# Kernel optimization log

Measured on AMD Instinct MI355X. Metric: run time of the kernel, lower is better.

Reference implementation:

```python
import jax, jax.numpy as jnp
import numpy as np

B, D_IN, D, E = 65536, 512, 512, 8  # batch, input dim, node hidden dim, n_children (=decision dim)


def setup_inputs() -> dict:
    key = jax.random.key(0)
    ks = jax.random.split(key, 5)
    s = 0.02  # weight init scale
    return {
        "x": jax.random.normal(ks[0], (B, D_IN), jnp.float32),
        "W_root": jax.random.normal(ks[1], (D_IN, D), jnp.float32) * s,
        "b_root": jnp.zeros((D,), jnp.float32),
        "W_dec": jax.random.normal(ks[2], (D, E), jnp.float32) * s,
        "b_dec": jnp.zeros((E,), jnp.float32),
        "W_leaf": jax.random.normal(ks[3], (E, D, D), jnp.float32) * s,
        "b_leaf": jnp.zeros((E, D), jnp.float32),
        "W_ldec": jax.random.normal(ks[4], (E, D, E), jnp.float32) * s,
        "b_ldec": jnp.zeros((E, E), jnp.float32),
    }


def reference(x, W_root, b_root, W_dec, b_dec, W_leaf, b_leaf, W_ldec, b_ldec):
    # Root node (Dense+relu), flatten is a no-op on [B, D]
    h = jax.nn.relu(x @ W_root + b_root)                                 # [B, D]
    dec = jax.nn.softmax(h @ W_dec + b_dec, axis=-1)                     # [B, E] root decision (softmax, outputDim>1)
    route = jnp.argmax(dec, axis=-1)                                     # [B] hard routing
    # Leaf children: each leaf applies its own node Dense+relu and decision Dense+softmax.
    # Dense reference for the boolean-mask dispatch/combine: compute all experts on all
    # samples, then gather each sample's routed expert output (math-equivalent to the
    # original gather-per-mask + concat + reorder-gather, since partitions are disjoint).
    lh = jax.nn.relu(jnp.einsum('bd,edh->ebh', h, W_leaf) + b_leaf[:, None, :])     # [E, B, D]
    ldec = jax.nn.softmax(jnp.einsum('ebd,edo->ebo', lh, W_ldec) + b_ldec[:, None, :], axis=-1)  # [E, B, E]
    sel = jnp.take_along_axis(ldec.transpose(1, 0, 2), route[:, None, None], axis=1)[:, 0]  # [B, E]
    # concat root decisionOut [B,1,E] with ordered leaf outputs [B,1,E] along axis -2
    return jnp.concatenate([dec[:, None, :], sel[:, None, :]], axis=1)  # [B, 2, E]
```

## Files before the change

### kernel.cpp

```cpp
#include <hip/hip_runtime.h>
#include <stdint.h>

#define DD   512
#define EE   8

typedef __bf16 bf16x8 __attribute__((ext_vector_type(8)));
typedef float  f32x4  __attribute__((ext_vector_type(4)));
typedef unsigned short u16x8 __attribute__((ext_vector_type(8)));

__device__ __forceinline__ unsigned short f2bf(float f) {
    union { float f; unsigned int i; } v; v.f = f;
    unsigned int x = v.i;
    x += 0x7fffu + ((x >> 16) & 1u);
    return (unsigned short)(x >> 16);
}
__device__ __forceinline__ void gload_lds16(const void* g, void* l) {
    __builtin_amdgcn_global_load_lds(
        (const __attribute__((address_space(1))) unsigned int*)g,
        (__attribute__((address_space(3))) unsigned int*)l, 16, 0, 0);
}
__device__ __forceinline__ f32x4 mfma_bf16(bf16x8 a, bf16x8 b, f32x4 c) {
    return __builtin_amdgcn_mfma_f32_16x16x32_bf16(a, b, c, 0, 0, 0);
}

__global__ __launch_bounds__(256) void k_wtr(
    const float* __restrict__ W_root, unsigned short* __restrict__ WrTh)
{
    __shared__ unsigned short tile[64][65];
    int tl = blockIdx.x, tr = tl >> 3, tc = tl & 7;
    int t = threadIdx.x;
    #pragma unroll
    for (int j = 0; j < 16; j++) {
        int i2 = t + j * 256; int r = i2 >> 6, c = i2 & 63;
        tile[r][c] = f2bf(W_root[(size_t)(tr * 64 + r) * DD + tc * 64 + c]);
    }
    __syncthreads();
    #pragma unroll
    for (int j = 0; j < 16; j++) {
        int i2 = t + j * 256; int r = i2 >> 6, c = i2 & 63;
        WrTh[(size_t)(tc * 64 + r) * DD + tr * 64 + c] = tile[c][r];
    }
}

__global__ __launch_bounds__(256) void k_trW(
    const float* __restrict__ W_leaf, unsigned short* __restrict__ WlT)
{
    __shared__ unsigned short tile[64][65];
    int bid = blockIdx.x;
    int e = bid >> 6;
    int tl = bid & 63, tr = tl >> 3, tc = tl & 7;
    const float* src = W_leaf + (size_t)e * DD * DD;
    unsigned short* dst = WlT + (size_t)e * DD * DD;
    int t = threadIdx.x;
    #pragma unroll
    for (int j = 0; j < 16; j++) {
        int i2 = t + j * 256; int r = i2 >> 6, c = i2 & 63;
        tile[r][c] = f2bf(src[(size_t)(tr * 64 + r) * DD + tc * 64 + c]);
    }
    __syncthreads();
    #pragma unroll
    for (int j = 0; j < 16; j++) {
        int i2 = t + j * 256; int r = i2 >> 6, c = i2 & 63;
        dst[(size_t)(tc * 64 + r) * DD + tr * 64 + c] = tile[c][r];
    }
}

__global__ __launch_bounds__(256) void k_trpad(
    const float* __restrict__ W_ldec, unsigned short* __restrict__ WldT)
{
    int idx = blockIdx.x * 256 + threadIdx.x;
    int e = idx >> 13, rem = idx & 8191;
    int o = rem >> 9, k = rem & 511;
    unsigned short v = 0;
    if (o < 8) v = f2bf(W_ldec[((size_t)e * DD + k) * EE + o]);
    WldT[idx] = v;
}

__global__ __launch_bounds__(256) void k_trdec(
    const float* __restrict__ W_dec, unsigned short* __restrict__ WdT)
{
    int idx = blockIdx.x * 256 + threadIdx.x;
    int o = idx >> 9, k = idx & 511;
    WdT[idx] = (o < 8) ? f2bf(W_dec[(size_t)k * EE + o]) : (unsigned short)0;
}

__global__ __launch_bounds__(256) void k_root(
    const float* __restrict__ x,
    const unsigned short* __restrict__ WrTh,
    const float* __restrict__ b_root,
    const unsigned short* __restrict__ WdT,
    unsigned short* __restrict__ hbuf,
    float* __restrict__ logit_part)
{
    __shared__ unsigned short smem[128 * 136];
    unsigned short* lsA = smem;
    unsigned short* lsB = smem + 4096;

    int bid = blockIdx.x;
    int mb = (bid >> 5) * 8 + (bid & 7);
    int cb = (bid >> 3) & 3;
    int m0 = mb * 128, n0 = cb * 128;

    int t = threadIdx.x;
    int wid = t >> 6, lane = t & 63;
    int wr = wid >> 1, wc = wid & 1;
    int l15 = lane & 15, l4 = lane >> 4;

    int ar = t >> 1, ah16 = (t & 1) * 16;
    const float* pA = x + (size_t)(m0 + ar) * DD + ah16;
    const unsigned short* srcB0 = WrTh + (size_t)(n0 + (t >> 2)) * DD + (t & 3) * 8;
    const unsigned short* srcB1 = srcB0 + (size_t)64 * DD;
    unsigned short* dB0 = &lsB[t * 8];
    unsigned short* dB1 = &lsB[2048 + t * 8];

    f32x4 acc[4][4];
    #pragma unroll
    for (int m = 0; m < 4; m++)
        #pragma unroll
        for (int n = 0; n < 4; n++) acc[m][n] = (f32x4){0.f, 0.f, 0.f, 0.f};

    for (int k0 = 0; k0 < DD; k0 += 32) {
        const float4* pAv = (const float4*)(pA + k0);
        float4 v0 = pAv[0], v1 = pAv[1], v2 = pAv[2], v3 = pAv[3];
        float vv[16] = {v0.x,v0.y,v0.z,v0.w, v1.x,v1.y,v1.z,v1.w,
                        v2.x,v2.y,v2.z,v2.w, v3.x,v3.y,v3.z,v3.w};
        bf16x8 hv0, hv1;
        #pragma unroll
        for (int j = 0; j < 8; j++) { hv0[j] = (__bf16)vv[j]; hv1[j] = (__bf16)vv[8 + j]; }
        __syncthreads();
        *(bf16x8*)&lsA[ar * 32 + ah16]     = hv0;
        *(bf16x8*)&lsA[ar * 32 + ah16 + 8] = hv1;
        gload_lds16(srcB0 + k0, dB0);
        gload_lds16(srcB1 + k0, dB1);
        __syncthreads();

        bf16x8 fa[4], fb[4];
        #pragma unroll
        for (int m = 0; m < 4; m++)
            fa[m] = *(const bf16x8*)&lsA[(wr * 64 + m * 16 + l15) * 32 + l4 * 8];
        #pragma unroll
        for (int n = 0; n < 4; n++)
            fb[n] = *(const bf16x8*)&lsB[(wc * 64 + n * 16 + l15) * 32 + l4 * 8];
        #pragma unroll
        for (int m = 0; m < 4; m++)
            #pragma unroll
            for (int n = 0; n < 4; n++)
                acc[m][n] = mfma_bf16(fa[m], fb[n], acc[m][n]);
    }
    __syncthreads();

    float bcol[4];
    #pragma unroll
    for (int n = 0; n < 4; n++) bcol[n] = b_root[n0 + wc * 64 + n * 16 + l15];
    #pragma unroll
    for (int n = 0; n < 4; n++) {
        int coll = wc * 64 + n * 16 + l15;
        #pragma unroll
        for (int m = 0; m < 4; m++) {
            int rl = wr * 64 + m * 16 + l4 * 4;
            #pragma unroll
            for (int i = 0; i < 4; i++) {
                float v = acc[m][n][i] + bcol[n];
                v = v > 0.f ? v : 0.f;
                smem[(rl + i) * 136 + coll] = f2bf(v);
            }
        }
    }
    __syncthreads();

    {
        int r = t >> 1, c0 = (t & 1) * 64;
        unsigned short* dst = hbuf + (size_t)(m0 + r) * DD + n0 + c0;
        #pragma unroll
        for (int j = 0; j < 8; j++)
            *(u16x8*)(dst + j * 8) = *(const u16x8*)&smem[r * 136 + c0 + j * 8];
    }

    f32x4 acc2[2];
    acc2[0] = (f32x4){0.f, 0.f, 0.f, 0.f};
    acc2[1] = (f32x4){0.f, 0.f, 0.f, 0.f};
    #pragma unroll
    for (int kk = 0; kk < 4; kk++) {
        bf16x8 bb = *(const bf16x8*)(WdT + (size_t)l15 * DD + n0 + kk * 32 + l4 * 8);
        #pragma unroll
        for (int m2 = 0; m2 < 2; m2++) {
            bf16x8 aa = *(const bf16x8*)&smem[(wid * 32 + m2 * 16 + l15) * 136 + kk * 32 + l4 * 8];
            acc2[m2] = mfma_bf16(aa, bb, acc2[m2]);
        }
    }
    if (l15 < 8) {
        #pragma unroll
        for (int m2 = 0; m2 < 2; m2++)
            #pragma unroll
            for (int i = 0; i < 4; i++) {
                int rowg = m0 + wid * 32 + m2 * 16 + l4 * 4 + i;
                logit_part[((size_t)cb * 65536 + rowg) * 8 + l15] = acc2[m2][i];
            }
    }
}

__global__ __launch_bounds__(256) void k_dec(
    const float* __restrict__ logit_part,
    const float* __restrict__ b_dec,
    float* __restrict__ out,
    int* __restrict__ route,
    int* __restrict__ meta,
    int* __restrict__ rescue_list)
{
    int b = blockIdx.x * 256 + threadIdx.x;
    double lg[8];
    #pragma unroll
    for (int o = 0; o < 8; o++) lg[o] = (double)b_dec[o];
    #pragma unroll
    for (int ppp = 0; ppp < 4; ppp++) {
        #pragma unroll
        for (int o = 0; o < 8; o++)
            lg[o] += (double)logit_part[((size_t)ppp * 65536 + b) * 8 + o];
    }
    double mx = -1e300, mx2 = -1e300; int idx = 0;
    #pragma unroll
    for (int o = 0; o < 8; o++) {
        if (lg[o] > mx) { mx2 = mx; mx = lg[o]; idx = o; }
        else if (lg[o] > mx2) mx2 = lg[o];
    }
    float ev[8], s = 0.f;
    #pragma unroll
    for (int o = 0; o < 8; o++) { ev[o] = expf((float)(lg[o] - mx)); s += ev[o]; }
    float inv = 1.f / s;
    float4 o0, o1;
    o0.x = ev[0]*inv; o0.y = ev[1]*inv; o0.z = ev[2]*inv; o0.w = ev[3]*inv;
    o1.x = ev[4]*inv; o1.y = ev[5]*inv; o1.z = ev[6]*inv; o1.w = ev[7]*inv;
    float4* op = (float4*)(out + (size_t)b * 16);
    op[0] = o0; op[1] = o1;
    route[b] = idx;
    if (mx - mx2 < 3e-3) {
        int pos = atomicAdd(&meta[27], 1);
        if (pos < 8192) rescue_list[pos] = b;
    }
}

__global__ __launch_bounds__(256) void k_rescue(
    const float* __restrict__ x,
    const float* __restrict__ W_root,
    const float* __restrict__ b_root,
    const float* __restrict__ W_dec,
    const float* __restrict__ b_dec,
    const int* __restrict__ rescue_list,
    const int* __restrict__ meta,
    float* __restrict__ out,
    int* __restrict__ route)
{
    int nresc = min(meta[27], 8192);
    if ((int)blockIdx.x >= nresc) return;
    int row = rescue_list[blockIdx.x];
    int t = threadIdx.x;

    __shared__ float xr[512];
    __shared__ double red[4][8];
    xr[t * 2]     = x[(size_t)row * DD + t * 2];
    xr[t * 2 + 1] = x[(size_t)row * DD + t * 2 + 1];
    __syncthreads();

    int d0 = t, d1 = t + 256;
    double a0 = 0.0, a1 = 0.0;
    for (int k = 0; k < DD; k++) {
        double xv = (double)xr[k];
        a0 += xv * (double)W_root[(size_t)k * DD + d0];
        a1 += xv * (double)W_root[(size_t)k * DD + d1];
    }
    double h0 = fmax(a0 + (double)b_root[d0], 0.0);
    double h1 = fmax(a1 + (double)b_root[d1], 0.0);
    double so[8];
    #pragma unroll
    for (int o = 0; o < 8; o++)
        so[o] = h0 * (double)W_dec[d0 * 8 + o] + h1 * (double)W_dec[d1 * 8 + o];
    #pragma unroll
    for (int d = 1; d < 64; d <<= 1)
        #pragma unroll
        for (int o = 0; o < 8; o++) so[o] += __shfl_xor(so[o], d, 64);
    if ((t & 63) == 0) {
        #pragma unroll
        for (int o = 0; o < 8; o++) red[t >> 6][o] = so[o];
    }
    __syncthreads();
    if (t == 0) {
        double lg[8]; double mx = -1e300; int idx = 0;
        #pragma unroll
        for (int o = 0; o < 8; o++) {
            lg[o] = red[0][o] + red[1][o] + red[2][o] + red[3][o] + (double)b_dec[o];
            if (lg[o] > mx) { mx = lg[o]; idx = o; }
        }
        double ev[8], s = 0.0;
        #pragma unroll
        for (int o = 0; o < 8; o++) { ev[o] = exp(lg[o] - mx); s += ev[o]; }
        double inv = 1.0 / s;
        float4 o0, o1;
        o0.x = (float)(ev[0]*inv); o0.y = (float)(ev[1]*inv);
        o0.z = (float)(ev[2]*inv); o0.w = (float)(ev[3]*inv);
        o1.x = (float)(ev[4]*inv); o1.y = (float)(ev[5]*inv);
        o1.z = (float)(ev[6]*inv); o1.w = (float)(ev[7]*inv);
        float4* op = (float4*)(out + (size_t)row * 16);
        op[0] = o0; op[1] = o1;
        route[row] = idx;
    }
}

__global__ __launch_bounds__(256) void k_count(
    const int* __restrict__ route, int* __restrict__ meta)
{
    __shared__ int wcnt[4][8];
    int b = blockIdx.x * 256 + threadIdx.x;
    int e = route[b];
    int lane = threadIdx.x & 63, wv = threadIdx.x >> 6;
    #pragma unroll
    for (int ex = 0; ex < 8; ex++) {
        unsigned long long m = __ballot(e == ex);
        if (lane == 0) wcnt[wv][ex] = __popcll(m);
    }
    __syncthreads();
    if (threadIdx.x < 8) {
        int ex = threadIdx.x;
        atomicAdd(&meta[ex], wcnt[0][ex] + wcnt[1][ex] + wcnt[2][ex] + wcnt[3][ex]);
    }
}

__global__ void k_scan(int* __restrict__ meta)
{
    if (threadIdx.x == 0 && blockIdx.x == 0) {
        int run = 0, rb = 0;
        for (int e = 0; e < 8; e++) {
            int c = meta[e];
            meta[16 + e] = run;
            meta[8 + e]  = run;
            int n = (c + 127) >> 7;
            for (int j = 0; j < n; j++) meta[32 + rb + j] = e | (j << 8);
            rb += n;
            run += n << 7;
        }
        meta[24] = rb;
    }
}

__global__ __launch_bounds__(256) void k_scatter(
    const int* __restrict__ route, int* __restrict__ meta, int* __restrict__ rows_list)
{
    __shared__ int wcnt[4][8];
    __shared__ int wbase[4][8];
    int b = blockIdx.x * 256 + threadIdx.x;
    int e = route[b];
    int lane = threadIdx.x & 63, wv = threadIdx.x >> 6;
    unsigned long long mymask = 0;
    #pragma unroll
    for (int ex = 0; ex < 8; ex++) {
        unsigned long long m = __ballot(e == ex);
        if (e == ex) mymask = m;
        if (lane == 0) wcnt[wv][ex] = __popcll(m);
    }
    int myrank = __popcll(mymask & ((1ULL << lane) - 1ULL));
    __syncthreads();
    if (threadIdx.x < 8) {
        int ex = threadIdx.x;
        int c0 = wcnt[0][ex], c1 = wcnt[1][ex], c2 = wcnt[2][ex], c3 = wcnt[3][ex];
        int base = atomicAdd(&meta[8 + ex], c0 + c1 + c2 + c3);
        wbase[0][ex] = base;
        wbase[1][ex] = base + c0;
        wbase[2][ex] = base + c0 + c1;
        wbase[3][ex] = base + c0 + c1 + c2;
    }
    __syncthreads();
    rows_list[wbase[wv][e] + myrank] = b;
}

__global__ __launch_bounds__(256) void k_gemm2(
    const unsigned short* __restrict__ hbuf,
    const unsigned short* __restrict__ WlT,
    const float* __restrict__ b_leaf,
    const unsigned short* __restrict__ WldT,
    const int* __restrict__ rows_list,
    const int* __restrict__ meta,
    float* __restrict__ ldec_part)
{
    __shared__ unsigned short lsA[128 * 32];
    __shared__ unsigned short lsB[128 * 32];
    __shared__ unsigned short lh[128 * 136];

    int bid = blockIdx.x;
    int rbid = (bid >> 5) * 8 + (bid & 7);
    int cb = (bid >> 3) & 3;
    if (rbid >= meta[24]) return;
    int pk = meta[32 + rbid];
    int e = pk & 255, lrb = pk >> 8;
    int poff_e = meta[16 + e], cnt_e = meta[e];
    int n0 = cb * 128;

    int t = threadIdx.x;
    int wid = t >> 6, lane = t & 63;
    int wr = wid >> 1, wc = wid & 1;
    int l15 = lane & 15, l4 = lane >> 4;

    int slot0 = poff_e + lrb * 128 + (t >> 2);
    int slot1 = slot0 + 64;
    int lastv = poff_e + cnt_e - 1;
    int grow0 = rows_list[min(slot0, lastv)];
    int grow1 = rows_list[min(slot1, lastv)];
    const unsigned short* srcA0 = hbuf + (size_t)grow0 * DD + (t & 3) * 8;
    const unsigned short* srcA1 = hbuf + (size_t)grow1 * DD + (t & 3) * 8;
    const unsigned short* srcB0 = WlT + (size_t)e * DD * DD + (size_t)(n0 + (t >> 2)) * DD + (t & 3) * 8;
    const unsigned short* srcB1 = srcB0 + (size_t)64 * DD;
    unsigned short* dA0 = &lsA[t * 8];
    unsigned short* dA1 = &lsA[2048 + t * 8];
    unsigned short* dB0 = &lsB[t * 8];
    unsigned short* dB1 = &lsB[2048 + t * 8];

    f32x4 acc[4][4];
    #pragma unroll
    for (int m = 0; m < 4; m++)
        #pragma unroll
        for (int n = 0; n < 4; n++) acc[m][n] = (f32x4){0.f, 0.f, 0.f, 0.f};

    for (int k0 = 0; k0 < DD; k0 += 32) {
        __syncthreads();
        gload_lds16(srcA0 + k0, dA0);
        gload_lds16(srcA1 + k0, dA1);
        gload_lds16(srcB0 + k0, dB0);
        gload_lds16(srcB1 + k0, dB1);
        __syncthreads();
        bf16x8 af[4], bfr[4];
        #pragma unroll
        for (int m = 0; m < 4; m++)
            af[m] = *(const bf16x8*)&lsA[(wr * 64 + m * 16 + l15) * 32 + l4 * 8];
        #pragma unroll
        for (int n = 0; n < 4; n++)
            bfr[n] = *(const bf16x8*)&lsB[(wc * 64 + n * 16 + l15) * 32 + l4 * 8];
        #pragma unroll
        for (int m = 0; m < 4; m++)
            #pragma unroll
            for (int n = 0; n < 4; n++)
                acc[m][n] = mfma_bf16(af[m], bfr[n], acc[m][n]);
    }

    #pragma unroll
    for (int n = 0; n < 4; n++) {
        int coll = wc * 64 + n * 16 + l15;
        float bv = b_leaf[(size_t)e * DD + n0 + coll];
        #pragma unroll
        for (int m = 0; m < 4; m++) {
            int rl = wr * 64 + m * 16 + l4 * 4;
            #pragma unroll
            for (int i = 0; i < 4; i++) {
                float v = acc[m][n][i] + bv;
                v = v > 0.f ? v : 0.f;
                lh[(rl + i) * 136 + coll] = f2bf(v);
            }
        }
    }
    __syncthreads();

    f32x4 acc2[2];
    acc2[0] = (f32x4){0.f, 0.f, 0.f, 0.f};
    acc2[1] = (f32x4){0.f, 0.f, 0.f, 0.f};
    #pragma unroll
    for (int kk = 0; kk < 4; kk++) {
        bf16x8 bb = *(const bf16x8*)(WldT + ((size_t)e * 16 + l15) * DD + n0 + kk * 32 + l4 * 8);
        #pragma unroll
        for (int m2 = 0; m2 < 2; m2++) {
            bf16x8 aa = *(const bf16x8*)&lh[(wid * 32 + m2 * 16 + l15) * 136 + kk * 32 + l4 * 8];
            acc2[m2] = mfma_bf16(aa, bb, acc2[m2]);
        }
    }
    if (l15 < 8) {
        #pragma unroll
        for (int m2 = 0; m2 < 2; m2++)
            #pragma unroll
            for (int i = 0; i < 4; i++) {
                int rl = wid * 32 + m2 * 16 + l4 * 4 + i;
                int s = min(poff_e + lrb * 128 + rl, lastv);
                int brow = rows_list[s];
                ldec_part[((size_t)cb * 65536 + brow) * 8 + l15] = acc2[m2][i];
            }
    }
}

__global__ __launch_bounds__(256) void k_sel(
    const float* __restrict__ ldec_part,
    const int* __restrict__ route,
    const float* __restrict__ b_ldec,
    float* __restrict__ out)
{
    int b = blockIdx.x * 256 + threadIdx.x;
    int e = route[b];
    float lg[8];
    #pragma unroll
    for (int o = 0; o < 8; o++) lg[o] = b_ldec[e * 8 + o];
    #pragma unroll
    for (int p = 0; p < 4; p++) {
        const float4* ap = (const float4*)(ldec_part + ((size_t)p * 65536 + b) * 8);
        float4 a0 = ap[0], a1 = ap[1];
        lg[0]+=a0.x; lg[1]+=a0.y; lg[2]+=a0.z; lg[3]+=a0.w;
        lg[4]+=a1.x; lg[5]+=a1.y; lg[6]+=a1.z; lg[7]+=a1.w;
    }
    float mx = -1e30f;
    #pragma unroll
    for (int o = 0; o < 8; o++) mx = fmaxf(mx, lg[o]);
    float ev[8], s = 0.f;
    #pragma unroll
    for (int o = 0; o < 8; o++) { ev[o] = expf(lg[o] - mx); s += ev[o]; }
    float inv = 1.f / s;
    float4 o0, o1;
    o0.x = ev[0]*inv; o0.y = ev[1]*inv; o0.z = ev[2]*inv; o0.w = ev[3]*inv;
    o1.x = ev[4]*inv; o1.y = ev[5]*inv; o1.z = ev[6]*inv; o1.w = ev[7]*inv;
    float4* op = (float4*)(out + (size_t)b * 16 + 8);
    op[0] = o0; op[1] = o1;
}

extern "C" void kernel_launch(void* const* d_in, const int* in_sizes, int n_in,
                              void* d_out, int out_size, void* d_ws, size_t ws_size,
                              hipStream_t stream)
{
    const float* x      = (const float*)d_in[0];
    const float* W_root = (const float*)d_in[1];
    const float* b_root = (const float*)d_in[2];
    const float* W_dec  = (const float*)d_in[3];
    const float* b_dec  = (const float*)d_in[4];
    const float* W_leaf = (const float*)d_in[5];
    const float* b_leaf = (const float*)d_in[6];
    const float* W_ldec = (const float*)d_in[7];
    const float* b_ldec = (const float*)d_in[8];
    float* out = (float*)d_out;

    char* w = (char*)d_ws;
    unsigned short* hbuf       = (unsigned short*)(w);
    float*          logit_part = (float*)(w + 67108864);
    unsigned short* WlT        = (unsigned short*)(w + 75497472);
    unsigned short* WldT       = (unsigned short*)(w + 79691776);
    unsigned short* WdT        = (unsigned short*)(w + 79822848);
    float*          ldec_part  = (float*)(w + 79839232);
    int*            route      = (int*)(w + 88227840);
    int*            rows_list  = (int*)(w + 88489984);
    unsigned short* WrTh       = (unsigned short*)(w + 88756224);
    int*            rescue     = (int*)(w + 89280512);
    int*            meta       = (int*)(w + 89313280);
    const size_t WS_NEED = 89317376ULL;
    if (ws_size < WS_NEED) return;

    hipMemsetAsync(meta, 0, 4096, stream);

    k_wtr    <<<64,   256, 0, stream>>>(W_root, WrTh);
    k_trW    <<<512,  256, 0, stream>>>(W_leaf, WlT);
    k_trpad  <<<256,  256, 0, stream>>>(W_ldec, WldT);
    k_trdec  <<<32,   256, 0, stream>>>(W_dec, WdT);
    k_root   <<<2048, 256, 0, stream>>>(x, WrTh, b_root, WdT, hbuf, logit_part);
    k_dec    <<<256,  256, 0, stream>>>(logit_part, b_dec, out, route, meta, rescue);
    k_rescue <<<8192, 256, 0, stream>>>(x, W_root, b_root, W_dec, b_dec, rescue, meta, out, route);
    k_count  <<<256,  256, 0, stream>>>(route, meta);
    k_scan   <<<1,    64,  0, stream>>>(meta);
    k_scatter<<<256,  256, 0, stream>>>(route, meta, rows_list);
    k_gemm2  <<<2080, 256, 0, stream>>>(hbuf, WlT, b_leaf, WldT, rows_list, meta, ldec_part);
    k_sel    <<<256,  256, 0, stream>>>(ldec_part, route, b_ldec, out);
}
```

Measured before the change: 275.3 us.

## Swizzle LDS tiles to avoid bank conflicts and prefetch root x tile

Applies an XOR swizzle to the K-chunk slot for the tiles written to LDS via direct global-to-LDS loads, in both the root GEMM (B operand) and the leaf expert GEMM (A and B operands). The fragment reads use the matching swizzle, which is meant to cut LDS bank conflicts on the MFMA operand loads. The root GEMM's x tile is padded to a row stride of 36, and the next x chunk is loaded into registers one iteration ahead to hide global latency. The register prefetch raises register pressure, and the padding shifts the LDS layout offsets.

```diff
diff --git a/kernel.cpp b/kernel.cpp
--- a/kernel.cpp
+++ b/kernel.cpp
@@ -94,7 +94,7 @@
 {
     __shared__ unsigned short smem[128 * 136];
     unsigned short* lsA = smem;
-    unsigned short* lsB = smem + 4096;
+    unsigned short* lsB = smem + 4608;
 
     int bid = blockIdx.x;
     int mb = (bid >> 5) * 8 + (bid & 7);
@@ -108,7 +108,8 @@
 
     int ar = t >> 1, ah16 = (t & 1) * 16;
     const float* pA = x + (size_t)(m0 + ar) * DD + ah16;
-    const unsigned short* srcB0 = WrTh + (size_t)(n0 + (t >> 2)) * DD + (t & 3) * 8;
+    int bslot = ((t & 3) ^ ((t >> 3) & 3)) * 8;
+    const unsigned short* srcB0 = WrTh + (size_t)(n0 + (t >> 2)) * DD + bslot;
     const unsigned short* srcB1 = srcB0 + (size_t)64 * DD;
     unsigned short* dB0 = &lsB[t * 8];
     unsigned short* dB1 = &lsB[2048 + t * 8];
@@ -119,17 +120,26 @@
         #pragma unroll
         for (int n = 0; n < 4; n++) acc[m][n] = (f32x4){0.f, 0.f, 0.f, 0.f};
 
+    float4 nv0, nv1, nv2, nv3;
+    {
+        const float4* p0 = (const float4*)pA;
+        nv0 = p0[0]; nv1 = p0[1]; nv2 = p0[2]; nv3 = p0[3];
+    }
+
     for (int k0 = 0; k0 < DD; k0 += 32) {
-        const float4* pAv = (const float4*)(pA + k0);
-        float4 v0 = pAv[0], v1 = pAv[1], v2 = pAv[2], v3 = pAv[3];
-        float vv[16] = {v0.x,v0.y,v0.z,v0.w, v1.x,v1.y,v1.z,v1.w,
-                        v2.x,v2.y,v2.z,v2.w, v3.x,v3.y,v3.z,v3.w};
+        float4 c0 = nv0, c1 = nv1, c2 = nv2, c3 = nv3;
+        if (k0 + 32 < DD) {
+            const float4* pn = (const float4*)(pA + k0 + 32);
+            nv0 = pn[0]; nv1 = pn[1]; nv2 = pn[2]; nv3 = pn[3];
+        }
+        float vv[16] = {c0.x,c0.y,c0.z,c0.w, c1.x,c1.y,c1.z,c1.w,
+                        c2.x,c2.y,c2.z,c2.w, c3.x,c3.y,c3.z,c3.w};
         bf16x8 hv0, hv1;
         #pragma unroll
         for (int j = 0; j < 8; j++) { hv0[j] = (__bf16)vv[j]; hv1[j] = (__bf16)vv[8 + j]; }
         __syncthreads();
-        *(bf16x8*)&lsA[ar * 32 + ah16]     = hv0;
-        *(bf16x8*)&lsA[ar * 32 + ah16 + 8] = hv1;
+        *(bf16x8*)&lsA[ar * 36 + ah16]     = hv0;
+        *(bf16x8*)&lsA[ar * 36 + ah16 + 8] = hv1;
         gload_lds16(srcB0 + k0, dB0);
         gload_lds16(srcB1 + k0, dB1);
         __syncthreads();
@@ -137,10 +147,12 @@
         bf16x8 fa[4], fb[4];
         #pragma unroll
         for (int m = 0; m < 4; m++)
-            fa[m] = *(const bf16x8*)&lsA[(wr * 64 + m * 16 + l15) * 32 + l4 * 8];
-        #pragma unroll
-        for (int n = 0; n < 4; n++)
-            fb[n] = *(const bf16x8*)&lsB[(wc * 64 + n * 16 + l15) * 32 + l4 * 8];
+            fa[m] = *(const bf16x8*)&lsA[(wr * 64 + m * 16 + l15) * 36 + l4 * 8];
+        #pragma unroll
+        for (int n = 0; n < 4; n++) {
+            int rb = wc * 64 + n * 16 + l15;
+            fb[n] = *(const bf16x8*)&lsB[rb * 32 + (l4 ^ ((rb >> 1) & 3)) * 8];
+        }
         #pragma unroll
         for (int m = 0; m < 4; m++)
             #pragma unroll
@@ -169,11 +181,11 @@
     __syncthreads();
 
     {
-        int r = t >> 1, c0 = (t & 1) * 64;
-        unsigned short* dst = hbuf + (size_t)(m0 + r) * DD + n0 + c0;
+        int r = t >> 1, c0s = (t & 1) * 64;
+        unsigned short* dst = hbuf + (size_t)(m0 + r) * DD + n0 + c0s;
         #pragma unroll
         for (int j = 0; j < 8; j++)
-            *(u16x8*)(dst + j * 8) = *(const u16x8*)&smem[r * 136 + c0 + j * 8];
+            *(u16x8*)(dst + j * 8) = *(const u16x8*)&smem[r * 136 + c0s + j * 8];
     }
 
     f32x4 acc2[2];
@@ -403,9 +415,10 @@
     int lastv = poff_e + cnt_e - 1;
     int grow0 = rows_list[min(slot0, lastv)];
     int grow1 = rows_list[min(slot1, lastv)];
-    const unsigned short* srcA0 = hbuf + (size_t)grow0 * DD + (t & 3) * 8;
-    const unsigned short* srcA1 = hbuf + (size_t)grow1 * DD + (t & 3) * 8;
-    const unsigned short* srcB0 = WlT + (size_t)e * DD * DD + (size_t)(n0 + (t >> 2)) * DD + (t & 3) * 8;
+    int kslot = ((t & 3) ^ ((t >> 3) & 3)) * 8;
+    const unsigned short* srcA0 = hbuf + (size_t)grow0 * DD + kslot;
+    const unsigned short* srcA1 = hbuf + (size_t)grow1 * DD + kslot;
+    const unsigned short* srcB0 = WlT + (size_t)e * DD * DD + (size_t)(n0 + (t >> 2)) * DD + kslot;
     const unsigned short* srcB1 = srcB0 + (size_t)64 * DD;
     unsigned short* dA0 = &lsA[t * 8];
     unsigned short* dA1 = &lsA[2048 + t * 8];
@@ -427,11 +440,15 @@
         __syncthreads();
         bf16x8 af[4], bfr[4];
         #pragma unroll
-        for (int m = 0; m < 4; m++)
-            af[m] = *(const bf16x8*)&lsA[(wr * 64 + m * 16 + l15) * 32 + l4 * 8];
-        #pragma unroll
-        for (int n = 0; n < 4; n++)
-            bfr[n] = *(const bf16x8*)&lsB[(wc * 64 + n * 16 + l15) * 32 + l4 * 8];
+        for (int m = 0; m < 4; m++) {
+            int ra = wr * 64 + m * 16 + l15;
+            af[m] = *(const bf16x8*)&lsA[ra * 32 + (l4 ^ ((ra >> 1) & 3)) * 8];
+        }
+        #pragma unroll
+        for (int n = 0; n < 4; n++) {
+            int rb = wc * 64 + n * 16 + l15;
+            bfr[n] = *(const bf16x8*)&lsB[rb * 32 + (l4 ^ ((rb >> 1) & 3)) * 8];
+        }
         #pragma unroll
         for (int m = 0; m < 4; m++)
             #pragma unroll
```

New measurement: 308.5 us. +12.1%, slower.

## Double-buffer LDS loads in root and leaf GEMMs with async global-to-LDS

Applied to the files above, without the earlier changes.

Both GEMM main loops now use two LDS buffers and prefetch the next K-slice with global_load_lds while MFMAs run on the current slice, cutting one barrier per iteration. In the root GEMM the fp32 x tile is loaded straight into LDS through direct loads with an XOR swizzle, and converted to bf16 when fragments are read, rather than converted in registers before an LDS store. The leaf kernel folds its three shared arrays into one aliased buffer and hoists the bias loads. This raises LDS use in the root kernel (48KB), which may lower occupancy and adds conversion work per fragment read.

```diff
diff --git a/kernel.cpp b/kernel.cpp
--- a/kernel.cpp
+++ b/kernel.cpp
@@ -92,9 +92,9 @@
     unsigned short* __restrict__ hbuf,
     float* __restrict__ logit_part)
 {
-    __shared__ unsigned short smem[128 * 136];
-    unsigned short* lsA = smem;
-    unsigned short* lsB = smem + 4096;
+    __shared__ unsigned short smem[24576];
+    float* fA = (float*)&smem[0];
+    unsigned short* bB = &smem[16384];
 
     int bid = blockIdx.x;
     int mb = (bid >> 5) * 8 + (bid & 7);
@@ -106,12 +106,12 @@
     int wr = wid >> 1, wc = wid & 1;
     int l15 = lane & 15, l4 = lane >> 4;
 
-    int ar = t >> 1, ah16 = (t & 1) * 16;
-    const float* pA = x + (size_t)(m0 + ar) * DD + ah16;
+    int arow = t >> 3;
+    int aswz = ((t & 7) ^ (arow & 7)) * 4;
+    const float* srcA = x + (size_t)(m0 + arow) * DD + aswz;
+    int adst = arow * 32 + aswz;
     const unsigned short* srcB0 = WrTh + (size_t)(n0 + (t >> 2)) * DD + (t & 3) * 8;
     const unsigned short* srcB1 = srcB0 + (size_t)64 * DD;
-    unsigned short* dB0 = &lsB[t * 8];
-    unsigned short* dB1 = &lsB[2048 + t * 8];
 
     f32x4 acc[4][4];
     #pragma unroll
@@ -119,35 +119,46 @@
         #pragma unroll
         for (int n = 0; n < 4; n++) acc[m][n] = (f32x4){0.f, 0.f, 0.f, 0.f};
 
-    for (int k0 = 0; k0 < DD; k0 += 32) {
-        const float4* pAv = (const float4*)(pA + k0);
-        float4 v0 = pAv[0], v1 = pAv[1], v2 = pAv[2], v3 = pAv[3];
-        float vv[16] = {v0.x,v0.y,v0.z,v0.w, v1.x,v1.y,v1.z,v1.w,
-                        v2.x,v2.y,v2.z,v2.w, v3.x,v3.y,v3.z,v3.w};
-        bf16x8 hv0, hv1;
-        #pragma unroll
-        for (int j = 0; j < 8; j++) { hv0[j] = (__bf16)vv[j]; hv1[j] = (__bf16)vv[8 + j]; }
-        __syncthreads();
-        *(bf16x8*)&lsA[ar * 32 + ah16]     = hv0;
-        *(bf16x8*)&lsA[ar * 32 + ah16 + 8] = hv1;
-        gload_lds16(srcB0 + k0, dB0);
-        gload_lds16(srcB1 + k0, dB1);
-        __syncthreads();
-
+    #pragma unroll
+    for (int j = 0; j < 4; j++)
+        gload_lds16(srcA + (size_t)j * 32 * DD, fA + adst + j * 1024);
+    gload_lds16(srcB0, bB + t * 8);
+    gload_lds16(srcB1, bB + 2048 + t * 8);
+    __syncthreads();
+
+    for (int it = 0; it < 16; ++it) {
+        int cur = it & 1;
+        int ao = cur * 4096;
+        int bo = cur * 4096;
+        if (it < 15) {
+            int k0n = (it + 1) * 32;
+            int aon = (cur ^ 1) * 4096, bon = (cur ^ 1) * 4096;
+            #pragma unroll
+            for (int j = 0; j < 4; j++)
+                gload_lds16(srcA + (size_t)j * 32 * DD + k0n, fA + aon + adst + j * 1024);
+            gload_lds16(srcB0 + k0n, bB + bon + t * 8);
+            gload_lds16(srcB1 + k0n, bB + bon + 2048 + t * 8);
+        }
         bf16x8 fa[4], fb[4];
         #pragma unroll
-        for (int m = 0; m < 4; m++)
-            fa[m] = *(const bf16x8*)&lsA[(wr * 64 + m * 16 + l15) * 32 + l4 * 8];
+        for (int m = 0; m < 4; m++) {
+            int r = wr * 64 + m * 16 + l15;
+            int s0 = (l4 * 2) ^ (r & 7), s1 = (l4 * 2 + 1) ^ (r & 7);
+            f32x4 lo = *(const f32x4*)&fA[ao + r * 32 + s0 * 4];
+            f32x4 hi = *(const f32x4*)&fA[ao + r * 32 + s1 * 4];
+            #pragma unroll
+            for (int j = 0; j < 4; j++) { fa[m][j] = (__bf16)lo[j]; fa[m][4 + j] = (__bf16)hi[j]; }
+        }
         #pragma unroll
         for (int n = 0; n < 4; n++)
-            fb[n] = *(const bf16x8*)&lsB[(wc * 64 + n * 16 + l15) * 32 + l4 * 8];
+            fb[n] = *(const bf16x8*)&bB[bo + (wc * 64 + n * 16 + l15) * 32 + l4 * 8];
         #pragma unroll
         for (int m = 0; m < 4; m++)
             #pragma unroll
             for (int n = 0; n < 4; n++)
                 acc[m][n] = mfma_bf16(fa[m], fb[n], acc[m][n]);
-    }
-    __syncthreads();
+        __syncthreads();
+    }
 
     float bcol[4];
     #pragma unroll
@@ -169,11 +180,11 @@
     __syncthreads();
 
     {
-        int r = t >> 1, c0 = (t & 1) * 64;
-        unsigned short* dst = hbuf + (size_t)(m0 + r) * DD + n0 + c0;
+        int r = t >> 1, c0s = (t & 1) * 64;
+        unsigned short* dst = hbuf + (size_t)(m0 + r) * DD + n0 + c0s;
         #pragma unroll
         for (int j = 0; j < 8; j++)
-            *(u16x8*)(dst + j * 8) = *(const u16x8*)&smem[r * 136 + c0 + j * 8];
+            *(u16x8*)(dst + j * 8) = *(const u16x8*)&smem[r * 136 + c0s + j * 8];
     }
 
     f32x4 acc2[2];
@@ -380,9 +391,7 @@
     const int* __restrict__ meta,
     float* __restrict__ ldec_part)
 {
-    __shared__ unsigned short lsA[128 * 32];
-    __shared__ unsigned short lsB[128 * 32];
-    __shared__ unsigned short lh[128 * 136];
+    __shared__ unsigned short smem[17408];
 
     int bid = blockIdx.x;
     int rbid = (bid >> 5) * 8 + (bid & 7);
@@ -407,10 +416,6 @@
     const unsigned short* srcA1 = hbuf + (size_t)grow1 * DD + (t & 3) * 8;
     const unsigned short* srcB0 = WlT + (size_t)e * DD * DD + (size_t)(n0 + (t >> 2)) * DD + (t & 3) * 8;
     const unsigned short* srcB1 = srcB0 + (size_t)64 * DD;
-    unsigned short* dA0 = &lsA[t * 8];
-    unsigned short* dA1 = &lsA[2048 + t * 8];
-    unsigned short* dB0 = &lsB[t * 8];
-    unsigned short* dB1 = &lsB[2048 + t * 8];
 
     f32x4 acc[4][4];
     #pragma unroll
@@ -418,39 +423,52 @@
         #pragma unroll
         for (int n = 0; n < 4; n++) acc[m][n] = (f32x4){0.f, 0.f, 0.f, 0.f};
 
-    for (int k0 = 0; k0 < DD; k0 += 32) {
-        __syncthreads();
-        gload_lds16(srcA0 + k0, dA0);
-        gload_lds16(srcA1 + k0, dA1);
-        gload_lds16(srcB0 + k0, dB0);
-        gload_lds16(srcB1 + k0, dB1);
-        __syncthreads();
+    gload_lds16(srcA0, &smem[t * 8]);
+    gload_lds16(srcA1, &smem[2048 + t * 8]);
+    gload_lds16(srcB0, &smem[8192 + t * 8]);
+    gload_lds16(srcB1, &smem[8192 + 2048 + t * 8]);
+    __syncthreads();
+
+    for (int it = 0; it < 16; ++it) {
+        int cur = it & 1;
+        int ao = cur * 4096, bo = 8192 + cur * 4096;
+        if (it < 15) {
+            int k0n = (it + 1) * 32;
+            int aon = (cur ^ 1) * 4096, bon = 8192 + (cur ^ 1) * 4096;
+            gload_lds16(srcA0 + k0n, &smem[aon + t * 8]);
+            gload_lds16(srcA1 + k0n, &smem[aon + 2048 + t * 8]);
+            gload_lds16(srcB0 + k0n, &smem[bon + t * 8]);
+            gload_lds16(srcB1 + k0n, &smem[bon + 2048 + t * 8]);
+        }
         bf16x8 af[4], bfr[4];
         #pragma unroll
         for (int m = 0; m < 4; m++)
-            af[m] = *(const bf16x8*)&lsA[(wr * 64 + m * 16 + l15) * 32 + l4 * 8];
+            af[m] = *(const bf16x8*)&smem[ao + (wr * 64 + m * 16 + l15) * 32 + l4 * 8];
         #pragma unroll
         for (int n = 0; n < 4; n++)
-            bfr[n] = *(const bf16x8*)&lsB[(wc * 64 + n * 16 + l15) * 32 + l4 * 8];
+            bfr[n] = *(const bf16x8*)&smem[bo + (wc * 64 + n * 16 + l15) * 32 + l4 * 8];
         #pragma unroll
         for (int m = 0; m < 4; m++)
             #pragma unroll
             for (int n = 0; n < 4; n++)
                 acc[m][n] = mfma_bf16(af[m], bfr[n], acc[m][n]);
-    }
-
+        __syncthreads();
+    }
+
+    float bcol[4];
+    #pragma unroll
+    for (int n = 0; n < 4; n++) bcol[n] = b_leaf[(size_t)e * DD + n0 + wc * 64 + n * 16 + l15];
     #pragma unroll
     for (int n = 0; n < 4; n++) {
         int coll = wc * 64 + n * 16 + l15;
-        float bv = b_leaf[(size_t)e * DD + n0 + coll];
         #pragma unroll
         for (int m = 0; m < 4; m++) {
             int rl = wr * 64 + m * 16 + l4 * 4;
             #pragma unroll
             for (int i = 0; i < 4; i++) {
-                float v = acc[m][n][i] + bv;
+                float v = acc[m][n][i] + bcol[n];
                 v = v > 0.f ? v : 0.f;
-                lh[(rl + i) * 136 + coll] = f2bf(v);
+                smem[(rl + i) * 136 + coll] = f2bf(v);
             }
         }
     }
@@ -464,7 +482,7 @@
         bf16x8 bb = *(const bf16x8*)(WldT + ((size_t)e * 16 + l15) * DD + n0 + kk * 32 + l4 * 8);
         #pragma unroll
         for (int m2 = 0; m2 < 2; m2++) {
-            bf16x8 aa = *(const bf16x8*)&lh[(wid * 32 + m2 * 16 + l15) * 136 + kk * 32 + l4 * 8];
+            bf16x8 aa = *(const bf16x8*)&smem[(wid * 32 + m2 * 16 + l15) * 136 + kk * 32 + l4 * 8];
             acc2[m2] = mfma_bf16(aa, bb, acc2[m2]);
         }
     }
@@ -543,7 +561,7 @@
     const size_t WS_NEED = 89317376ULL;
     if (ws_size < WS_NEED) return;
 
-    hipMemsetAsync(meta, 0, 4096, stream);
+    (void)hipMemsetAsync(meta, 0, 4096, stream);
 
     k_wtr    <<<64,   256, 0, stream>>>(W_root, WrTh);
     k_trW    <<<512,  256, 0, stream>>>(W_leaf, WlT);
```

Measured after the change: 266.6 us. -3.2%, faster.
